# Performance work log

Measured on AMD Instinct MI355X. Metric: run time of the kernel, lower is better.

## Reference

```python
import jax, jax.numpy as jnp
import numpy as np

MAX_NUM_CENTERS = 100
CENTER_IGNORE_PX = 3
SIGMA = 2.0   # center_gt_blur
KSIZE = 21    # GaussianLayer kernel size (ReflectionPad2d(10) + Conv2d(k=21))


def _gauss_kernel():
    r = KSIZE // 2
    x = jnp.arange(-r, r + 1, dtype=jnp.float32)
    g = jnp.exp(-0.5 * (x / SIGMA) ** 2)
    g = g / g.sum()
    return jnp.outer(g, g)  # [21,21], sums to 1 (matches scipy gaussian_filter of a delta)


def _gaussian_blur(x):
    # x: [B,H,W] -> depthwise 21x21 gaussian with reflect padding (GaussianLayer)
    r = KSIZE // 2
    k = _gauss_kernel()[None, None]  # [1,1,21,21]
    xp = jnp.pad(x[:, None], ((0, 0), (0, 0), (r, r), (r, r)), mode="reflect")
    y = jax.lax.conv_general_dilated(xp, k, (1, 1), "VALID",
                                     dimension_numbers=("NCHW", "OIHW", "NCHW"))
    return y[:, 0]


def setup_inputs() -> dict:
    key = jax.random.key(0)
    k1, k2 = jax.random.split(key)
    B, H, W = 8, 768, 768
    instances = jax.random.randint(k1, (B, 1, H, W), 0, MAX_NUM_CENTERS, dtype=jnp.int32)
    centers = jax.random.uniform(k2, (B, MAX_NUM_CENTERS, 2), dtype=jnp.float32) * (H - 1) + 1.0
    return {"instances": instances, "centers": centers}


def reference(instances, centers):
    B, _, H, W = instances.shape
    inst = instances[:, 0]                                # [B,H,W]
    col = jnp.arange(W, dtype=jnp.float32)                # xym_s[0][i,j] = j
    row = jnp.arange(H, dtype=jnp.float32)[:, None]       # xym_s[1][i,j] = i

    valid = inst > 0                                      # instance_mask
    has_inst = jnp.any(valid, axis=(1, 2)).astype(jnp.float32)  # len(unique)>1 gate

    # per-pixel nearest-center gather: center = centers[b, id-1]
    idx = jnp.clip(inst - 1, 0, MAX_NUM_CENTERS - 1)
    c = centers[jnp.arange(B)[:, None, None], idx]        # [B,H,W,2]
    gt_cx = jnp.where(valid, c[..., 1], -10000.0)         # gt_center_x (swapped coords)
    gt_cy = jnp.where(valid, c[..., 0], -10000.0)

    gt_X = gt_cx - row                                    # gt_center_x - xym_s[1]
    gt_Y = gt_cy - col                                    # gt_center_y - xym_s[0]

    near = (jnp.abs(gt_X) < CENTER_IGNORE_PX) & (jnp.abs(gt_Y) < CENTER_IGNORE_PX)
    # batches with no instances skip the block -> ignore stays all-ones
    ignore = jnp.where(has_inst[:, None, None] > 0, (~near).astype(jnp.float32), 1.0)

    m = valid.astype(jnp.float32)
    R = jnp.sqrt(gt_X ** 2 + gt_Y ** 2) * m
    theta_raw = jnp.arctan2(gt_Y, gt_X)
    theta = theta_raw * has_inst[:, None, None]           # skipped (zero) when no instances
    s = jnp.sin(theta_raw) * m
    cth = jnp.cos(theta_raw) * m
    M = jnp.sqrt(s ** 2 + cth ** 2)                       # == m, kept for faithfulness
    s = jnp.where(valid, s / jnp.maximum(M, 1e-12), 0.0)
    cth = jnp.where(valid, cth / jnp.maximum(M, 1e-12), 0.0)

    # gt_center_mask: zeros if no center-neighborhood pixels, else normalized blur
    blur = _gaussian_blur(1.0 - ignore)
    all_ones = jnp.all(ignore >= 1.0, axis=(1, 2))        # gt_center_mask.all()
    bmax = jnp.max(blur, axis=(1, 2), keepdims=True)
    cmask = jnp.where(all_ones[:, None, None], 0.0, blur / jnp.maximum(bmax, 1e-12))

    top = jnp.stack([R, theta, s, cth, ignore, cmask], axis=1)       # [B,6,H,W]
    mat = jnp.concatenate([top, jnp.zeros((B, 7, H, W), top.dtype)], axis=1)[:, :, None]
    # mat: [B,13,1,H,W]; channels 6..12 are zero (no orientation input)

    # gt_centers[id] = centers[b, id-1][[1,0]] for each instance id present
    present = jnp.zeros((B, MAX_NUM_CENTERS), dtype=bool).at[
        jnp.arange(B)[:, None], inst.reshape(B, -1)].set(True)
    swapped = centers[..., ::-1]
    gt_centers = jnp.zeros_like(centers).at[:, 1:, :].set(
        jnp.where(present[:, 1:, None], swapped[:, :-1, :], 0.0))

    return mat, gt_centers
```

## Files before the change

### kernel.cpp

```cpp
#include <hip/hip_runtime.h>
#include <math.h>

#define NB 8
#define NH 768
#define NW 768
#define NHW (NH*NW)
#define NCEN 100
#define NPIX (NB*NHW)
#define RAD 10
#define KS 21

#define SCAN_BLKS (NPIX / 4096)
#define BLKS_PER_B (NHW / 4096)
#define QBLK_PER_B (NHW / 1024)
#define CAND_BLKS 96
#define MID_BLKS 2048
#define BSLOT 24
#define BCAP 23
#define GCAP 256
#define FCAP 256

#define OFF_MASKS 0
#define OFF_BLIST 4608
#define OFF_BMAXP 32256
#define OFF_HAS   33024
#define OFF_M     33032
#define OFF_GLIST 33040
#define WS_INTS   35088

typedef float f4 __attribute__((ext_vector_type(4)));

__device__ const float g_G[KS] = {
    7.4335e-7f, 7.9919e-6f, 6.6915e-5f, 0.00043634f, 0.00221592f,
    0.00876415f, 0.02699548f, 0.06475880f, 0.12098536f, 0.17603266f,
    0.19947114f,
    0.17603266f, 0.12098536f, 0.06475880f, 0.02699548f, 0.00876415f,
    0.00221592f, 0.00043634f, 6.6915e-5f, 7.9919e-6f, 7.4335e-7f};

__device__ __forceinline__ float wfun(int p, int q, const float* __restrict__ g) {
    int d = p - q;
    float w = 0.f;
    if (d >= -RAD && d <= RAD) w = g[d + RAD];
    int a = p + q;
    if (q > 0 && a <= RAD) w += g[a + RAD];
    if (q < NH - 1 && a >= 2 * (NH - 1) - RAD) w += g[a - 2 * (NH - 1) + RAD];
    return w;
}

__device__ __forceinline__ float fatan2(float Y, float X) {
    float ax = fabsf(X), ay = fabsf(Y);
    float mx = fmaxf(ax, ay), mn = fminf(ax, ay);
    float a = mx > 0.f ? __fdividef(mn, mx) : 0.f;
    float ss = a * a;
    float r = fmaf(fmaf(fmaf(fmaf(fmaf(-0.01172120f, ss, 0.05265332f), ss,
                -0.11643287f), ss, 0.19354346f), ss, -0.33262347f), ss, 0.99997726f) * a;
    if (ay > ax) r = 1.57079637f - r;
    if (X < 0.f) r = 3.14159274f - r;
    return copysignf(r, Y);
}

template <bool U8>
__global__ __launch_bounds__(256) void k_scan(const int4* __restrict__ inst4,
                                              const float* __restrict__ centers,
                                              int* __restrict__ ws,
                                              unsigned char* __restrict__ u8) {
    __shared__ unsigned sm[4];
    __shared__ float2 s_c2[NCEN];
    __shared__ int s_loc[BCAP];
    __shared__ int s_lcnt;
    int t = threadIdx.x;
    int blk = blockIdx.x;
    int b = blk / BLKS_PER_B;
    int lblk = blk - b * BLKS_PER_B;
    if (t < 4) sm[t] = 0;
    if (t == 0) s_lcnt = 0;
    for (int k = t; k < NCEN; k += 256)
        s_c2[k] = ((const float2*)centers)[b * NCEN + k];
    __syncthreads();

    unsigned m0 = 0, m1 = 0, m2 = 0, m3 = 0;
    size_t base = (size_t)blk * 1024 + t;
    int ppb = lblk * 4096 + t * 4;
#pragma unroll
    for (int q = 0; q < 4; q++) {
        int4 v = inst4[base + (size_t)q * 256];
        int pp = ppb + q * 1024;
        int i = pp / NW;
        int j0 = pp - i * NW;
        if (U8) {
            unsigned packed = ((unsigned)v.x & 255u) | (((unsigned)v.y & 255u) << 8) |
                              (((unsigned)v.z & 255u) << 16) | (((unsigned)v.w & 255u) << 24);
            *(unsigned*)&u8[(size_t)blk * 4096 + q * 1024 + t * 4] = packed;
        }
        int a[4] = {v.x, v.y, v.z, v.w};
#pragma unroll
        for (int e = 0; e < 4; e++) {
            int iv = a[e];
            if (iv > 0) {
                unsigned bit = 1u << (iv & 31);
                int w = iv >> 5;
                if (w == 0) m0 |= bit; else if (w == 1) m1 |= bit;
                else if (w == 2) m2 |= bit; else m3 |= bit;
                int idx = iv - 1;
                idx = idx > NCEN - 1 ? NCEN - 1 : idx;
                float2 c = s_c2[idx];
                if (fabsf(c.y - (float)i) < 3.f && fabsf(c.x - (float)(j0 + e)) < 3.f) {
                    int slot = atomicAdd(&s_lcnt, 1);
                    if (slot < BCAP) s_loc[slot] = (i << 16) | (j0 + e);
                }
            }
        }
    }
#pragma unroll
    for (int off = 32; off >= 1; off >>= 1) {
        m0 |= __shfl_xor(m0, off);
        m1 |= __shfl_xor(m1, off);
        m2 |= __shfl_xor(m2, off);
        m3 |= __shfl_xor(m3, off);
    }
    if ((t & 63) == 0) {
        if (m0) atomicOr(&sm[0], m0);
        if (m1) atomicOr(&sm[1], m1);
        if (m2) atomicOr(&sm[2], m2);
        if (m3) atomicOr(&sm[3], m3);
    }
    __syncthreads();
    if (t < 4) ws[OFF_MASKS + blk * 4 + t] = (int)sm[t];
    int cnt = s_lcnt < BCAP ? s_lcnt : BCAP;
    int* slot = &ws[OFF_BLIST + blk * BSLOT];
    if (t == 0) slot[0] = cnt;
    if (t < cnt) slot[1 + t] = s_loc[t];
}

__global__ __launch_bounds__(256) void k_mid(const float* __restrict__ centers,
                                             int* __restrict__ ws,
                                             float* __restrict__ out) {
    int t = threadIdx.x;
    int g = blockIdx.x;

    if (g < NB * CAND_BLKS) {
        __shared__ float s_g[KS];
        __shared__ int s_list[GCAP];
        __shared__ int s_tot;
        __shared__ unsigned s_m[4];
        __shared__ float s_red[4];
        int b = g / CAND_BLKS;
        int cb = g - b * CAND_BLKS;
        if (t < KS) s_g[t] = g_G[t];
        if (t == 0) s_tot = 0;
        if (t < 4) s_m[t] = 0;
        __syncthreads();
        if (t < BLKS_PER_B) {
            const int* slot = &ws[OFF_BLIST + (b * BLKS_PER_B + t) * BSLOT];
            int cnt = slot[0];
            cnt = cnt < 0 ? 0 : (cnt > BCAP ? BCAP : cnt);
            int basep = atomicAdd(&s_tot, cnt);
            for (int i2 = 0; i2 < cnt; i2++) {
                int s = basep + i2;
                if (s < GCAP) s_list[s] = slot[1 + i2];
            }
            if (cb == 0) {
                const unsigned* pm = (const unsigned*)&ws[OFF_MASKS + (b * BLKS_PER_B + t) * 4];
                unsigned w0 = pm[0], w1 = pm[1], w2 = pm[2], w3 = pm[3];
                if (w0) atomicOr(&s_m[0], w0);
                if (w1) atomicOr(&s_m[1], w1);
                if (w2) atomicOr(&s_m[2], w2);
                if (w3) atomicOr(&s_m[3], w3);
            }
        }
        __syncthreads();
        int M = s_tot < GCAP ? s_tot : GCAP;

        if (cb == 0) {
            float* gt = out + (size_t)NB * 13 * NHW;
            if (t < NCEN) {
                float vx = 0.f, vy = 0.f;
                if (t >= 1 && ((s_m[t >> 5] >> (t & 31)) & 1u)) {
                    vx = centers[(b * NCEN + (t - 1)) * 2 + 1];
                    vy = centers[(b * NCEN + (t - 1)) * 2 + 0];
                }
                gt[(b * NCEN + t) * 2 + 0] = vx;
                gt[(b * NCEN + t) * 2 + 1] = vy;
            }
            if (t == 0) {
                unsigned any = (s_m[0] & 0xFFFFFFFEu) | s_m[1] | s_m[2] | s_m[3];
                ws[OFF_HAS + b] = any ? 1 : 0;
                ws[OFF_M + b] = M;
            }
            for (int e = t; e < M; e += 256) ws[OFF_GLIST + b * GCAP + e] = s_list[e];
        }

        float lmax = 0.f;
        int total = M * (KS * KS);
        for (int c = cb * 256 + t; c < total; c += CAND_BLKS * 256) {
            int m = c / (KS * KS), r = c - m * (KS * KS);
            int e = s_list[m];
            int pi = (e >> 16) + r / KS - RAD;
            int pj = (e & 0xFFFF) + (r - (r / KS) * KS) - RAD;
            if (pi < 0 || pi >= NH || pj < 0 || pj >= NW) continue;
            float acc = 0.f;
            for (int m2 = 0; m2 < M; m2++) {
                int e2 = s_list[m2];
                float wi = wfun(pi, e2 >> 16, s_g);
                if (wi == 0.f) continue;
                acc += wi * wfun(pj, e2 & 0xFFFF, s_g);
            }
            lmax = fmaxf(lmax, acc);
        }
#pragma unroll
        for (int off = 32; off >= 1; off >>= 1) lmax = fmaxf(lmax, __shfl_down(lmax, off));
        if ((t & 63) == 0) s_red[t >> 6] = lmax;
        __syncthreads();
        if (t == 0) {
            float bmx = fmaxf(fmaxf(s_red[0], s_red[1]), fmaxf(s_red[2], s_red[3]));
            ((float*)ws)[OFF_BMAXP + b * CAND_BLKS + cb] = bmx;
        }
    }

    const int CH7Q = 7 * NHW / 4;
    const int ZTOT = NB * CH7Q;
    f4 z = {0.f, 0.f, 0.f, 0.f};
    for (int zi = g * 256 + t; zi < ZTOT; zi += MID_BLKS * 256) {
        int b2 = zi / CH7Q;
        int rem = zi - b2 * CH7Q;
        size_t off = (size_t)b2 * (13 * NHW / 4) + (6 * NHW / 4) + rem;
        __builtin_nontemporal_store(z, (f4*)out + off);
    }
}

template <bool U8>
__global__ __launch_bounds__(256) void k_fused(const int* __restrict__ inst,
                                               const unsigned char* __restrict__ u8,
                                               const float* __restrict__ centers,
                                               const int* __restrict__ ws,
                                               float* __restrict__ out) {
    __shared__ float s_cen[2 * NCEN];
    __shared__ float s_g[KS];
    __shared__ int s_fl[FCAP];
    __shared__ int s_fM;
    __shared__ unsigned s_bm;
    int t = threadIdx.x;
    int b = blockIdx.x / QBLK_PER_B;
    int qblk = blockIdx.x - b * QBLK_PER_B;

    int has = ws[OFF_HAS + b];
    int M = ws[OFF_M + b];
    for (int k = t; k < 2 * NCEN; k += 256) s_cen[k] = centers[b * 2 * NCEN + k];
    if (t < KS) s_g[t] = g_G[t];
    if (t == 255) s_fM = 0;
    if (t == 254) s_bm = 0;
    __syncthreads();

    if (t < CAND_BLKS)
        atomicMax(&s_bm, __float_as_uint(((const float*)ws)[OFF_BMAXP + b * CAND_BLKS + t]));

    int p0blk = qblk * 1024;
    int r0 = p0blk / NW;
    const int* gl = &ws[OFF_GLIST + b * GCAP];
    for (int m = t; m < M; m += 256) {
        int e = gl[m];
        int qi = e >> 16;
        if (wfun(r0, qi, s_g) != 0.f || wfun(r0 + 1, qi, s_g) != 0.f) {
            int slot = atomicAdd(&s_fM, 1);
            if (slot < FCAP) s_fl[slot] = e;
        }
    }
    __syncthreads();
    int FM = s_fM < FCAP ? s_fM : FCAP;
    float bmx = __uint_as_float(s_bm);
    float sc = (has && M > 0) ? 1.f / fmaxf(bmx, 1e-12f) : 0.f;

    int p0 = p0blk + t * 4;
    int gi = p0 / NW;
    int gj0 = p0 - gi * NW;
    float* outb = out + (size_t)b * 13 * NHW;

    int ia[4];
    if (U8) {
        unsigned v8 = *(const unsigned*)&u8[(size_t)b * NHW + p0];
        ia[0] = v8 & 255; ia[1] = (v8 >> 8) & 255; ia[2] = (v8 >> 16) & 255; ia[3] = v8 >> 24;
    } else {
        int4 ivv = *(const int4*)&inst[(size_t)b * NHW + p0];
        ia[0] = ivv.x; ia[1] = ivv.y; ia[2] = ivv.z; ia[3] = ivv.w;
    }
    f4 vR, vTh, vS, vC, vIg;
#pragma unroll
    for (int e = 0; e < 4; e++) {
        int iv = ia[e];
        bool valid = iv > 0;
        int idx = iv - 1;
        idx = idx < 0 ? 0 : idx;
        float cy = s_cen[2 * idx];
        float cx = s_cen[2 * idx + 1];
        float gcx = valid ? cx : -10000.f;
        float gcy = valid ? cy : -10000.f;
        float X = gcx - (float)gi;
        float Y = gcy - (float)(gj0 + e);
        bool near = (fabsf(X) < 3.f) && (fabsf(Y) < 3.f);
        vIg[e] = (has != 0) ? (near ? 0.f : 1.f) : 1.f;
        float m = valid ? 1.f : 0.f;
        float R2 = X * X + Y * Y;
        vR[e] = sqrtf(R2) * m;
        float rinv = R2 > 0.f ? rsqrtf(R2) : 0.f;
        vS[e] = valid ? Y * rinv : 0.f;
        vC[e] = valid ? (R2 > 0.f ? X * rinv : 1.f) : 0.f;
        float th = fatan2(Y, X);
        vTh[e] = (has != 0) ? th : 0.f;
    }

    f4 blur = {0.f, 0.f, 0.f, 0.f};
    for (int m = 0; m < FM; m++) {
        int e2 = s_fl[m];
        float wi = wfun(gi, e2 >> 16, s_g);
        if (wi == 0.f) continue;
        int qj = e2 & 0xFFFF;
#pragma unroll
        for (int e = 0; e < 4; e++) blur[e] += wi * wfun(gj0 + e, qj, s_g);
    }
    f4 vCm = blur * sc;

    __builtin_nontemporal_store(vR,  (f4*)&outb[(size_t)0 * NHW + p0]);
    __builtin_nontemporal_store(vTh, (f4*)&outb[(size_t)1 * NHW + p0]);
    __builtin_nontemporal_store(vS,  (f4*)&outb[(size_t)2 * NHW + p0]);
    __builtin_nontemporal_store(vC,  (f4*)&outb[(size_t)3 * NHW + p0]);
    __builtin_nontemporal_store(vIg, (f4*)&outb[(size_t)4 * NHW + p0]);
    __builtin_nontemporal_store(vCm, (f4*)&outb[(size_t)5 * NHW + p0]);
}

extern "C" void kernel_launch(void* const* d_in, const int* in_sizes, int n_in,
                              void* d_out, int out_size, void* d_ws, size_t ws_size,
                              hipStream_t stream) {
    const int* inst = (const int*)d_in[0];
    const float* centers = (const float*)d_in[1];
    float* out = (float*)d_out;
    int* ws = (int*)d_ws;
    unsigned char* u8 = (unsigned char*)d_ws + (size_t)WS_INTS * 4;
    bool use_u8 = ws_size >= (size_t)WS_INTS * 4 + (size_t)NPIX;

    if (use_u8) {
        k_scan<true><<<SCAN_BLKS, 256, 0, stream>>>((const int4*)inst, centers, ws, u8);
        k_mid<<<MID_BLKS, 256, 0, stream>>>(centers, ws, out);
        k_fused<true><<<NB * QBLK_PER_B, 256, 0, stream>>>(inst, u8, centers, ws, out);
    } else {
        k_scan<false><<<SCAN_BLKS, 256, 0, stream>>>((const int4*)inst, centers, ws, u8);
        k_mid<<<MID_BLKS, 256, 0, stream>>>(centers, ws, out);
        k_fused<false><<<NB * QBLK_PER_B, 256, 0, stream>>>(inst, u8, centers, ws, out);
    }
}
```

Baseline: 270.1 us.

## Process three 1024-pixel chunks per fused block and restructure zero-fill blocks

The fused kernel now covers 3072 pixels (four image rows) per block. The per-block setup work (loading centers, reducing the blur max, filtering the candidate list) is paid once for three chunks instead of once per chunk. The zero channels are now written by dedicated blocks in k_mid, each doing fixed contiguous unrolled stores, instead of a grid-stride loop run by every block. k_scan stages the packed u8 labels in shared memory and writes them out as 16-byte vectors. The cost is fewer fused blocks, hence less parallelism, and a candidate filter that now checks four rows per entry.

```diff
diff --git a/kernel.cpp b/kernel.cpp
--- a/kernel.cpp
+++ b/kernel.cpp
@@ -12,9 +12,14 @@
 
 #define SCAN_BLKS (NPIX / 4096)
 #define BLKS_PER_B (NHW / 4096)
-#define QBLK_PER_B (NHW / 1024)
 #define CAND_BLKS 96
-#define MID_BLKS 2048
+#define ZBLKS 1344
+#define ZPB 6144
+#define ZBLK_PER_B 168
+#define MID_BLKS (NB*CAND_BLKS + ZBLKS)
+#define NPQ 3
+#define FBLK_PX (NPQ*1024)
+#define QBLK3_PER_B (NHW / FBLK_PX)
 #define BSLOT 24
 #define BCAP 23
 #define GCAP 256
@@ -68,6 +73,7 @@
     __shared__ float2 s_c2[NCEN];
     __shared__ int s_loc[BCAP];
     __shared__ int s_lcnt;
+    __shared__ unsigned s_u8[1024];
     int t = threadIdx.x;
     int blk = blockIdx.x;
     int b = blk / BLKS_PER_B;
@@ -90,7 +96,7 @@
         if (U8) {
             unsigned packed = ((unsigned)v.x & 255u) | (((unsigned)v.y & 255u) << 8) |
                               (((unsigned)v.z & 255u) << 16) | (((unsigned)v.w & 255u) << 24);
-            *(unsigned*)&u8[(size_t)blk * 4096 + q * 1024 + t * 4] = packed;
+            s_u8[q * 256 + t] = packed;
         }
         int a[4] = {v.x, v.y, v.z, v.w};
 #pragma unroll
@@ -125,6 +131,10 @@
         if (m3) atomicOr(&sm[3], m3);
     }
     __syncthreads();
+    if (U8) {
+        int4 vv = ((const int4*)s_u8)[t];
+        *(int4*)&u8[(size_t)blk * 4096 + t * 16] = vv;
+    }
     if (t < 4) ws[OFF_MASKS + blk * 4 + t] = (int)sm[t];
     int cnt = s_lcnt < BCAP ? s_lcnt : BCAP;
     int* slot = &ws[OFF_BLIST + blk * BSLOT];
@@ -215,16 +225,15 @@
             float bmx = fmaxf(fmaxf(s_red[0], s_red[1]), fmaxf(s_red[2], s_red[3]));
             ((float*)ws)[OFF_BMAXP + b * CAND_BLKS + cb] = bmx;
         }
-    }
-
-    const int CH7Q = 7 * NHW / 4;
-    const int ZTOT = NB * CH7Q;
-    f4 z = {0.f, 0.f, 0.f, 0.f};
-    for (int zi = g * 256 + t; zi < ZTOT; zi += MID_BLKS * 256) {
-        int b2 = zi / CH7Q;
-        int rem = zi - b2 * CH7Q;
-        size_t off = (size_t)b2 * (13 * NHW / 4) + (6 * NHW / 4) + rem;
-        __builtin_nontemporal_store(z, (f4*)out + off);
+    } else {
+        int zblk = g - NB * CAND_BLKS;
+        int b2 = zblk / ZBLK_PER_B;
+        int rem0 = (zblk - b2 * ZBLK_PER_B) * ZPB;
+        f4 z = {0.f, 0.f, 0.f, 0.f};
+        f4* dst = (f4*)out + (size_t)b2 * (13 * NHW / 4) + (6 * NHW / 4) + rem0 + t;
+#pragma unroll
+        for (int it = 0; it < ZPB / 256; ++it)
+            __builtin_nontemporal_store(z, dst + it * 256);
     }
 }
 
@@ -240,8 +249,8 @@
     __shared__ int s_fM;
     __shared__ unsigned s_bm;
     int t = threadIdx.x;
-    int b = blockIdx.x / QBLK_PER_B;
-    int qblk = blockIdx.x - b * QBLK_PER_B;
+    int b = blockIdx.x / QBLK3_PER_B;
+    int qblk = blockIdx.x - b * QBLK3_PER_B;
 
     int has = ws[OFF_HAS + b];
     int M = ws[OFF_M + b];
@@ -254,13 +263,16 @@
     if (t < CAND_BLKS)
         atomicMax(&s_bm, __float_as_uint(((const float*)ws)[OFF_BMAXP + b * CAND_BLKS + t]));
 
-    int p0blk = qblk * 1024;
-    int r0 = p0blk / NW;
+    int p0blk = qblk * FBLK_PX;
+    int r0 = qblk * 4;
     const int* gl = &ws[OFF_GLIST + b * GCAP];
     for (int m = t; m < M; m += 256) {
         int e = gl[m];
         int qi = e >> 16;
-        if (wfun(r0, qi, s_g) != 0.f || wfun(r0 + 1, qi, s_g) != 0.f) {
+        bool keep = false;
+#pragma unroll
+        for (int rr = 0; rr < 4; rr++) keep |= (wfun(r0 + rr, qi, s_g) != 0.f);
+        if (keep) {
             int slot = atomicAdd(&s_fM, 1);
             if (slot < FCAP) s_fl[slot] = e;
         }
@@ -270,61 +282,64 @@
     float bmx = __uint_as_float(s_bm);
     float sc = (has && M > 0) ? 1.f / fmaxf(bmx, 1e-12f) : 0.f;
 
-    int p0 = p0blk + t * 4;
-    int gi = p0 / NW;
-    int gj0 = p0 - gi * NW;
     float* outb = out + (size_t)b * 13 * NHW;
 
-    int ia[4];
-    if (U8) {
-        unsigned v8 = *(const unsigned*)&u8[(size_t)b * NHW + p0];
-        ia[0] = v8 & 255; ia[1] = (v8 >> 8) & 255; ia[2] = (v8 >> 16) & 255; ia[3] = v8 >> 24;
-    } else {
-        int4 ivv = *(const int4*)&inst[(size_t)b * NHW + p0];
-        ia[0] = ivv.x; ia[1] = ivv.y; ia[2] = ivv.z; ia[3] = ivv.w;
-    }
-    f4 vR, vTh, vS, vC, vIg;
-#pragma unroll
-    for (int e = 0; e < 4; e++) {
-        int iv = ia[e];
-        bool valid = iv > 0;
-        int idx = iv - 1;
-        idx = idx < 0 ? 0 : idx;
-        float cy = s_cen[2 * idx];
-        float cx = s_cen[2 * idx + 1];
-        float gcx = valid ? cx : -10000.f;
-        float gcy = valid ? cy : -10000.f;
-        float X = gcx - (float)gi;
-        float Y = gcy - (float)(gj0 + e);
-        bool near = (fabsf(X) < 3.f) && (fabsf(Y) < 3.f);
-        vIg[e] = (has != 0) ? (near ? 0.f : 1.f) : 1.f;
-        float m = valid ? 1.f : 0.f;
-        float R2 = X * X + Y * Y;
-        vR[e] = sqrtf(R2) * m;
-        float rinv = R2 > 0.f ? rsqrtf(R2) : 0.f;
-        vS[e] = valid ? Y * rinv : 0.f;
-        vC[e] = valid ? (R2 > 0.f ? X * rinv : 1.f) : 0.f;
-        float th = fatan2(Y, X);
-        vTh[e] = (has != 0) ? th : 0.f;
-    }
-
-    f4 blur = {0.f, 0.f, 0.f, 0.f};
-    for (int m = 0; m < FM; m++) {
-        int e2 = s_fl[m];
-        float wi = wfun(gi, e2 >> 16, s_g);
-        if (wi == 0.f) continue;
-        int qj = e2 & 0xFFFF;
-#pragma unroll
-        for (int e = 0; e < 4; e++) blur[e] += wi * wfun(gj0 + e, qj, s_g);
-    }
-    f4 vCm = blur * sc;
-
-    __builtin_nontemporal_store(vR,  (f4*)&outb[(size_t)0 * NHW + p0]);
-    __builtin_nontemporal_store(vTh, (f4*)&outb[(size_t)1 * NHW + p0]);
-    __builtin_nontemporal_store(vS,  (f4*)&outb[(size_t)2 * NHW + p0]);
-    __builtin_nontemporal_store(vC,  (f4*)&outb[(size_t)3 * NHW + p0]);
-    __builtin_nontemporal_store(vIg, (f4*)&outb[(size_t)4 * NHW + p0]);
-    __builtin_nontemporal_store(vCm, (f4*)&outb[(size_t)5 * NHW + p0]);
+    for (int qq = 0; qq < NPQ; ++qq) {
+        int p0 = p0blk + qq * 1024 + t * 4;
+        int gi = p0 / NW;
+        int gj0 = p0 - gi * NW;
+
+        int ia[4];
+        if (U8) {
+            unsigned v8 = *(const unsigned*)&u8[(size_t)b * NHW + p0];
+            ia[0] = v8 & 255; ia[1] = (v8 >> 8) & 255; ia[2] = (v8 >> 16) & 255; ia[3] = v8 >> 24;
+        } else {
+            int4 ivv = *(const int4*)&inst[(size_t)b * NHW + p0];
+            ia[0] = ivv.x; ia[1] = ivv.y; ia[2] = ivv.z; ia[3] = ivv.w;
+        }
+        f4 vR, vTh, vS, vC, vIg;
+#pragma unroll
+        for (int e = 0; e < 4; e++) {
+            int iv = ia[e];
+            bool valid = iv > 0;
+            int idx = iv - 1;
+            idx = idx < 0 ? 0 : idx;
+            float cy = s_cen[2 * idx];
+            float cx = s_cen[2 * idx + 1];
+            float gcx = valid ? cx : -10000.f;
+            float gcy = valid ? cy : -10000.f;
+            float X = gcx - (float)gi;
+            float Y = gcy - (float)(gj0 + e);
+            bool near = (fabsf(X) < 3.f) && (fabsf(Y) < 3.f);
+            vIg[e] = (has != 0) ? (near ? 0.f : 1.f) : 1.f;
+            float m = valid ? 1.f : 0.f;
+            float R2 = X * X + Y * Y;
+            vR[e] = sqrtf(R2) * m;
+            float rinv = R2 > 0.f ? rsqrtf(R2) : 0.f;
+            vS[e] = valid ? Y * rinv : 0.f;
+            vC[e] = valid ? (R2 > 0.f ? X * rinv : 1.f) : 0.f;
+            float th = fatan2(Y, X);
+            vTh[e] = (has != 0) ? th : 0.f;
+        }
+
+        f4 blur = {0.f, 0.f, 0.f, 0.f};
+        for (int m = 0; m < FM; m++) {
+            int e2 = s_fl[m];
+            float wi = wfun(gi, e2 >> 16, s_g);
+            if (wi == 0.f) continue;
+            int qj = e2 & 0xFFFF;
+#pragma unroll
+            for (int e = 0; e < 4; e++) blur[e] += wi * wfun(gj0 + e, qj, s_g);
+        }
+        f4 vCm = blur * sc;
+
+        __builtin_nontemporal_store(vR,  (f4*)&outb[(size_t)0 * NHW + p0]);
+        __builtin_nontemporal_store(vTh, (f4*)&outb[(size_t)1 * NHW + p0]);
+        __builtin_nontemporal_store(vS,  (f4*)&outb[(size_t)2 * NHW + p0]);
+        __builtin_nontemporal_store(vC,  (f4*)&outb[(size_t)3 * NHW + p0]);
+        __builtin_nontemporal_store(vIg, (f4*)&outb[(size_t)4 * NHW + p0]);
+        __builtin_nontemporal_store(vCm, (f4*)&outb[(size_t)5 * NHW + p0]);
+    }
 }
 
 extern "C" void kernel_launch(void* const* d_in, const int* in_sizes, int n_in,
@@ -340,10 +355,10 @@
     if (use_u8) {
         k_scan<true><<<SCAN_BLKS, 256, 0, stream>>>((const int4*)inst, centers, ws, u8);
         k_mid<<<MID_BLKS, 256, 0, stream>>>(centers, ws, out);
-        k_fused<true><<<NB * QBLK_PER_B, 256, 0, stream>>>(inst, u8, centers, ws, out);
+        k_fused<true><<<NB * QBLK3_PER_B, 256, 0, stream>>>(inst, u8, centers, ws, out);
     } else {
         k_scan<false><<<SCAN_BLKS, 256, 0, stream>>>((const int4*)inst, centers, ws, u8);
         k_mid<<<MID_BLKS, 256, 0, stream>>>(centers, ws, out);
-        k_fused<false><<<NB * QBLK_PER_B, 256, 0, stream>>>(inst, u8, centers, ws, out);
-    }
-}
+        k_fused<false><<<NB * QBLK3_PER_B, 256, 0, stream>>>(inst, u8, centers, ws, out);
+    }
+}
```

After: 272.5 us. No clear change (+0.9%).
